# Kernel optimization log

Hardware: AMD Instinct MI355X
Metric: run time of the kernel (lower is better)

The kernel has to match this reference:

```python
import jax, jax.numpy as jnp
import numpy as np

B, T, D = 32, 512, 1024


def setup_inputs() -> dict:
    key = jax.random.key(0)
    ks = jax.random.split(key, 10)
    s = 1.0 / np.sqrt(D)
    return {
        "x": jax.random.normal(ks[0], (B, T, D), jnp.float32),
        "W1": jax.random.normal(ks[1], (D, D), jnp.float32) * s,
        "b1": jax.random.normal(ks[2], (D,), jnp.float32) * s,
        "W2": jax.random.normal(ks[3], (D, D), jnp.float32) * s,
        "b2": jax.random.normal(ks[4], (D,), jnp.float32) * s,
        "W3": jax.random.normal(ks[5], (D, D), jnp.float32) * s,
        "b3": jax.random.normal(ks[6], (D,), jnp.float32) * s,
        "W4": jax.random.normal(ks[7], (D, D), jnp.float32) * s,
        "b4": jax.random.normal(ks[8], (D,), jnp.float32) * s,
        "bias": jax.random.normal(ks[9], (1, D), jnp.float32),
    }


def _lstm(x, W1, b1, W2, b2, W3, b3, W4, b4, bias):
    # Fuse the four D->D gate projections into one [D,4D] matmul per step.
    # nn.Linear computes s @ W^T + b; weights here are stored as [out,in]=[D,D].
    Wcat = jnp.concatenate([W1.T, W2.T, W3.T, W4.T], axis=1)        # [D, 4D]
    bcat = jnp.concatenate([b1, b2, b3, b4]) + jnp.tile(bias[0], 4)  # [4D]

    def step(carry, xt):
        c, h = carry                      # cellState (hiddenUp), hidden (hiddenDown): [B,D]
        s = h + xt                        # sum_ = hiddenDown + xt
        z = s @ Wcat + bcat               # [B,4D]
        zf, zi, zg, zo = jnp.split(z, 4, axis=1)
        f = jax.nn.sigmoid(zf)            # forgetGate
        i = jax.nn.sigmoid(zi) * jnp.tanh(zg)  # inputGate
        c = c * f + i                     # cellUpdate
        h = jax.nn.sigmoid(zo) * jnp.tanh(c)   # outputGate -> hiddenDown
        return (c, h), h

    c0 = jnp.zeros((x.shape[0], x.shape[2]), x.dtype)
    h0 = jnp.zeros_like(c0)
    (cT, hT), ys = jax.lax.scan(step, (c0, h0), jnp.swapaxes(x, 0, 1))
    out = jnp.swapaxes(ys, 0, 1)          # [B,T,D]
    return out, cT[:, None, :], hT[:, None, :]


def reference(x, W1, b1, W2, b2, W3, b3, W4, b4, bias):
    return _lstm(x, W1, b1, W2, b2, W3, b3, W4, b4, bias)
```

## Files before the change

kernel.cpp:

```cpp
#include <hip/hip_runtime.h>
#include <hip/hip_bf16.h>

#define NBLK 64
#define NTHR 256

typedef __attribute__((ext_vector_type(8))) short short8;
typedef __attribute__((ext_vector_type(4))) float f32x4;

constexpr int B = 32, T = 512, D = 1024;
constexpr int JW = D / NBLK;
constexpr int KW = D / 4;
static_assert(JW * NBLK == D, "partition");


__device__ __forceinline__ unsigned short f2bf(float f) {
  unsigned u = __builtin_bit_cast(unsigned, f);
  u += 0x7FFFu + ((u >> 16) & 1u);
  return (unsigned short)(u >> 16);
}

__device__ __forceinline__ float sigm(float v) {
  return 1.0f / (1.0f + __expf(-v));
}

__device__ __forceinline__ float tanh_fast(float v) {
  v = fminf(fmaxf(v, -30.0f), 30.0f);
  float e = __expf(2.0f * v);
  return (e - 1.0f) / (e + 1.0f);
}

__device__ __forceinline__ void st_u32_llc(unsigned* p, unsigned v) {
  asm volatile("global_store_dword %0, %1, off sc0 sc1" :: "v"(p), "v"(v) : "memory");
}

struct u32x4s { unsigned x, y, z, w; };

__global__ void __launch_bounds__(NTHR, 1) lstm_persistent(
    const float* __restrict__ x,
    const float* __restrict__ W1, const float* __restrict__ b1,
    const float* __restrict__ W2, const float* __restrict__ b2,
    const float* __restrict__ W3, const float* __restrict__ b3,
    const float* __restrict__ W4, const float* __restrict__ b4,
    const float* __restrict__ bias,
    float* __restrict__ out,
    unsigned* __restrict__ flags,
    unsigned* __restrict__ sq)
{
  __shared__ float zx[2][4][B][72];

  const int blk  = blockIdx.x;
  const int tid  = threadIdx.x;
  const int wv   = tid >> 6;
  const int lane = tid & 63;
  const int j0   = blk * JW;
  const int rot  = blk & 7;

  const int m     = lane & 15;
  const int kg    = (lane >> 4) * 8;
  const int kbase = wv * KW;

  const float* Wg[4] = {W1, W2, W3, W4};
  short8 bfrag[4][8];
#pragma unroll
  for (int g = 0; g < 4; ++g) {
    const float* wrow = Wg[g] + (size_t)(j0 + m) * D + kbase;
#pragma unroll
    for (int kk = 0; kk < 8; ++kk) {
      const int kkr = (kk + rot) & 7;
      float4 fa = *(const float4*)(wrow + kkr * 32 + kg);
      float4 fb = *(const float4*)(wrow + kkr * 32 + kg + 4);
      short8 v;
      v[0] = (short)f2bf(fa.x); v[1] = (short)f2bf(fa.y);
      v[2] = (short)f2bf(fa.z); v[3] = (short)f2bf(fa.w);
      v[4] = (short)f2bf(fb.x); v[5] = (short)f2bf(fb.y);
      v[6] = (short)f2bf(fb.z); v[7] = (short)f2bf(fb.w);
      bfrag[g][kk] = v;
    }
  }

  const int gb   = tid >> 3;
  const int jp   = (tid & 7) * 2;
  const int jcol = j0 + jp;

  const float bsum0 = bias[jcol], bsum1 = bias[jcol + 1];
  const float bf0 = b1[jcol] + bsum0, bf1 = b1[jcol + 1] + bsum1;
  const float bi0 = b2[jcol] + bsum0, bi1 = b2[jcol + 1] + bsum1;
  const float bg0 = b3[jcol] + bsum0, bg1 = b3[jcol + 1] + bsum1;
  const float bo0 = b4[jcol] + bsum0, bo1 = b4[jcol + 1] + bsum1;

  const float* xrow = x + (size_t)gb * T * D + jcol;
  float* outrow     = out + (size_t)gb * T * D + jcol;
  float* cTp        = out + (size_t)B * T * D + (size_t)gb * D + jcol;
  float* hTp        = cTp + (size_t)B * D;

  {
    float2 x0 = *(const float2*)xrow;
    unsigned v = ((unsigned)f2bf(x0.x) | ((unsigned)f2bf(x0.y) << 16)) & ~1u;
    st_u32_llc(sq + blk * 256 + tid, v);
    asm volatile("s_waitcnt vmcnt(0)" ::: "memory");
    if (lane < 8) st_u32_llc(flags + lane * 256 + 4 * blk + wv, 1u);
  }

  const int aoff = ((kbase >> 4) + (kg >> 4)) * 512 + m * 16 + (kg & 8);
  const unsigned* pollp = flags + rot * 256 + 64 * wv + lane;

  float c0 = 0.0f, c1 = 0.0f;
  unsigned rA = 0, rB = 0;

  for (int t = 0; t < T; ++t) {
    const int tn = (t + 1 < T) ? (t + 1) : (T - 1);
    float2 xv;
    asm volatile("global_load_dwordx2 %0, %1, off"
                 : "=v"(xv) : "v"(xrow + (size_t)tn * D));

    {
      const unsigned tgt = (unsigned)(t + 1);
      int guard = 0;
      asm volatile("global_load_dword %0, %1, off sc0 sc1" : "=v"(rA) : "v"(pollp));
      for (;;) {
        asm volatile("global_load_dword %0, %1, off sc0 sc1" : "=v"(rB) : "v"(pollp));
        asm volatile("s_waitcnt vmcnt(1)" ::: "memory");
        __builtin_amdgcn_sched_barrier(0);
        if (__all((int)(rA >= tgt))) break;
        asm volatile("global_load_dword %0, %1, off sc0 sc1" : "=v"(rA) : "v"(pollp));
        asm volatile("s_waitcnt vmcnt(1)" ::: "memory");
        __builtin_amdgcn_sched_barrier(0);
        if (__all((int)(rB >= tgt))) break;
        if (++guard > (1 << 21)) break;
      }
    }
    __builtin_amdgcn_sched_barrier(0);

    const unsigned short* ap =
        (const unsigned short*)sq + (size_t)(t & 1) * 32768 + aoff;
    const unsigned eexp = (unsigned)(t >> 1) & 1u;
    short8 a0[8], a1[8];
    f32x4 acc[2][4];
    int atry = 0;
    bool good;
    do {
#pragma unroll
      for (int kk = 0; kk < 8; ++kk) {
        const int kkr = (kk + rot) & 7;
        asm volatile("global_load_dwordx4 %0, %1, off sc0 sc1"
                     : "=v"(a0[kk]) : "v"(ap + kkr * 1024));
        asm volatile("global_load_dwordx4 %0, %1, off sc0 sc1"
                     : "=v"(a1[kk]) : "v"(ap + kkr * 1024 + 256));
      }
#pragma unroll
      for (int mt = 0; mt < 2; ++mt)
#pragma unroll
        for (int g = 0; g < 4; ++g) acc[mt][g] = (f32x4){0.f, 0.f, 0.f, 0.f};

      unsigned orv = 0u, andv = 0xFFFFFFFFu;
#define MFMA_KK(kk, NSTR)                                                     \
      asm volatile("s_waitcnt vmcnt(" NSTR ")" ::: "memory");                 \
      __builtin_amdgcn_sched_barrier(0);                                      \
      _Pragma("unroll")                                                       \
      for (int g = 0; g < 4; ++g) {                                           \
        acc[0][g] = __builtin_amdgcn_mfma_f32_16x16x32_bf16(a0[kk], bfrag[g][kk], acc[0][g], 0, 0, 0); \
        acc[1][g] = __builtin_amdgcn_mfma_f32_16x16x32_bf16(a1[kk], bfrag[g][kk], acc[1][g], 0, 0, 0); \
      }                                                                       \
      {                                                                       \
        u32x4s q0 = __builtin_bit_cast(u32x4s, a0[kk]);                       \
        u32x4s q1 = __builtin_bit_cast(u32x4s, a1[kk]);                       \
        unsigned o_ = q0.x | q0.y | q0.z | q0.w | q1.x | q1.y | q1.z | q1.w;  \
        unsigned a_ = q0.x & q0.y & q0.z & q0.w & q1.x & q1.y & q1.z & q1.w;  \
        orv |= o_; andv &= a_;                                                \
      }
      MFMA_KK(0, "14") MFMA_KK(1, "12") MFMA_KK(2, "10") MFMA_KK(3, "8")
      MFMA_KK(4, "6")  MFMA_KK(5, "4")  MFMA_KK(6, "2")  MFMA_KK(7, "0")
#undef MFMA_KK
      const unsigned bad = eexp ? (~andv & 1u) : (orv & 1u);
      good = __all((int)(bad == 0u));
    } while (!good && ++atry < 64);

    const int pz = t & 1;
    {
      const int zr = (lane >> 4) * 4;
#pragma unroll
      for (int g = 0; g < 4; ++g)
#pragma unroll
        for (int r = 0; r < 4; ++r) {
          zx[pz][wv][zr + r][g * 16 + m]      = acc[0][g][r];
          zx[pz][wv][zr + r + 16][g * 16 + m] = acc[1][g][r];
        }
    }
    __syncthreads();

    float zf0, zf1, zi0, zi1, zg0, zg1, zo0, zo1;
    {
      float2 f_ = *(const float2*)&zx[pz][0][gb][jp];
      float2 i_ = *(const float2*)&zx[pz][0][gb][16 + jp];
      float2 g_ = *(const float2*)&zx[pz][0][gb][32 + jp];
      float2 o_ = *(const float2*)&zx[pz][0][gb][48 + jp];
      zf0 = f_.x; zf1 = f_.y; zi0 = i_.x; zi1 = i_.y;
      zg0 = g_.x; zg1 = g_.y; zo0 = o_.x; zo1 = o_.y;
#pragma unroll
      for (int w = 1; w < 4; ++w) {
        f_ = *(const float2*)&zx[pz][w][gb][jp];
        i_ = *(const float2*)&zx[pz][w][gb][16 + jp];
        g_ = *(const float2*)&zx[pz][w][gb][32 + jp];
        o_ = *(const float2*)&zx[pz][w][gb][48 + jp];
        zf0 += f_.x; zf1 += f_.y; zi0 += i_.x; zi1 += i_.y;
        zg0 += g_.x; zg1 += g_.y; zo0 += o_.x; zo1 += o_.y;
      }
    }

    float f0 = sigm(zf0 + bf0), f1 = sigm(zf1 + bf1);
    float i0 = sigm(zi0 + bi0) * tanh_fast(zg0 + bg0);
    float i1 = sigm(zi1 + bi1) * tanh_fast(zg1 + bg1);
    c0 = c0 * f0 + i0;
    c1 = c1 * f1 + i1;
    float h0 = sigm(zo0 + bo0) * tanh_fast(c0);
    float h1 = sigm(zo1 + bo1) * tanh_fast(c1);

    if (t + 1 < T) {
      const unsigned epub = (unsigned)((t + 1) >> 1) & 1u;
      unsigned v = (((unsigned)f2bf(h0 + xv.x) |
                     ((unsigned)f2bf(h1 + xv.y) << 16)) & ~1u) | epub;
      st_u32_llc(sq + (size_t)((t + 1) & 1) * 16384 + blk * 256 + tid, v);
      if (lane < 8) st_u32_llc(flags + lane * 256 + 4 * blk + wv, (unsigned)(t + 2));
      *(float2*)(outrow + (size_t)t * D) = make_float2(h0, h1);
    } else {
      *(float2*)(outrow + (size_t)t * D) = make_float2(h0, h1);
      *(float2*)cTp = make_float2(c0, c1);
      *(float2*)hTp = make_float2(h0, h1);
    }

    asm volatile("" :: "v"(rA), "v"(rB), "v"(xv));
  }
}

extern "C" void kernel_launch(void* const* d_in, const int* in_sizes, int n_in,
                              void* d_out, int out_size, void* d_ws, size_t ws_size,
                              hipStream_t stream) {
  const float* x    = (const float*)d_in[0];
  const float* W1   = (const float*)d_in[1];
  const float* b1   = (const float*)d_in[2];
  const float* W2   = (const float*)d_in[3];
  const float* b2   = (const float*)d_in[4];
  const float* W3   = (const float*)d_in[5];
  const float* b3   = (const float*)d_in[6];
  const float* W4   = (const float*)d_in[7];
  const float* b4   = (const float*)d_in[8];
  const float* bias = (const float*)d_in[9];

  unsigned* flags = (unsigned*)d_ws;
  unsigned* sq    = (unsigned*)((char*)d_ws + 8192);

  hipMemsetAsync(d_ws, 0, 8192, stream);
  hipMemsetAsync((char*)d_ws + 8192, 0xFF, 131072, stream);
  hipLaunchKernelGGL(lstm_persistent, dim3(NBLK), dim3(NTHR), 0, stream,
                     x, W1, b1, W2, b2, W3, b3, W4, b4, bias,
                     (float*)d_out, flags, sq);
}
```

Before: 1.691 ms.

## Replace flag polling with double-buffered data polling using embedded epoch bits

Removes the separate per-step flag array and its polling loop. Each block now speculatively issues two rounds of loads of the shared hidden-state buffer and checks the epoch bit embedded in every bf16 pair, retrying until one set is complete, then runs the MFMAs on that set. This removes one global round-trip (flag store and flag poll) from the serial critical path of each timestep. In exchange it roughly doubles the vector registers held for operands and adds more L2 polling traffic. An odd `zo0*0.0f` term is also added to h1, which looks like a scheduling nudge and changes nothing numerically for finite inputs.

```diff
diff --git a/kernel.cpp b/kernel.cpp
--- a/kernel.cpp
+++ b/kernel.cpp
@@ -34,6 +34,30 @@
 }
 
 struct u32x4s { unsigned x, y, z, w; };
+
+__device__ __forceinline__ int check_set(const short8* a0, const short8* a1,
+                                         unsigned eexp) {
+  unsigned r;
+  if (eexp) {
+    r = 0xFFFFFFFFu;
+#pragma unroll
+    for (int kk = 0; kk < 8; ++kk) {
+      u32x4s q0 = __builtin_bit_cast(u32x4s, a0[kk]);
+      u32x4s q1 = __builtin_bit_cast(u32x4s, a1[kk]);
+      r &= q0.x & q0.y & q0.z & q0.w & q1.x & q1.y & q1.z & q1.w;
+    }
+    return __all((int)(r & 1u));
+  } else {
+    r = 0u;
+#pragma unroll
+    for (int kk = 0; kk < 8; ++kk) {
+      u32x4s q0 = __builtin_bit_cast(u32x4s, a0[kk]);
+      u32x4s q1 = __builtin_bit_cast(u32x4s, a1[kk]);
+      r |= q0.x | q0.y | q0.z | q0.w | q1.x | q1.y | q1.z | q1.w;
+    }
+    return __all((int)((r & 1u) == 0u));
+  }
+}
 
 __global__ void __launch_bounds__(NTHR, 1) lstm_persistent(
     const float* __restrict__ x,
@@ -43,7 +67,6 @@
     const float* __restrict__ W4, const float* __restrict__ b4,
     const float* __restrict__ bias,
     float* __restrict__ out,
-    unsigned* __restrict__ flags,
     unsigned* __restrict__ sq)
 {
   __shared__ float zx[2][4][B][72];
@@ -97,15 +120,35 @@
     float2 x0 = *(const float2*)xrow;
     unsigned v = ((unsigned)f2bf(x0.x) | ((unsigned)f2bf(x0.y) << 16)) & ~1u;
     st_u32_llc(sq + blk * 256 + tid, v);
-    asm volatile("s_waitcnt vmcnt(0)" ::: "memory");
-    if (lane < 8) st_u32_llc(flags + lane * 256 + 4 * blk + wv, 1u);
   }
 
   const int aoff = ((kbase >> 4) + (kg >> 4)) * 512 + m * 16 + (kg & 8);
-  const unsigned* pollp = flags + rot * 256 + 64 * wv + lane;
 
   float c0 = 0.0f, c1 = 0.0f;
-  unsigned rA = 0, rB = 0;
+  short8 a0A[8], a1A[8], a0B[8], a1B[8];
+
+#define ISSUE_SET(A0, A1)                                                     \
+  do {                                                                        \
+    _Pragma("unroll")                                                         \
+    for (int kk = 0; kk < 8; ++kk) {                                          \
+      const int kkr = (kk + rot) & 7;                                         \
+      asm volatile("global_load_dwordx4 %0, %1, off sc0 sc1"                  \
+                   : "=v"((A0)[kk]) : "v"(ap + kkr * 1024));                  \
+      asm volatile("global_load_dwordx4 %0, %1, off sc0 sc1"                  \
+                   : "=v"((A1)[kk]) : "v"(ap + kkr * 1024 + 256));            \
+    }                                                                         \
+  } while (0)
+
+#define MFMA_ALL(A0, A1)                                                      \
+  do {                                                                        \
+    _Pragma("unroll")                                                         \
+    for (int kk = 0; kk < 8; ++kk)                                            \
+      _Pragma("unroll")                                                       \
+      for (int g = 0; g < 4; ++g) {                                           \
+        acc[0][g] = __builtin_amdgcn_mfma_f32_16x16x32_bf16((A0)[kk], bfrag[g][kk], acc[0][g], 0, 0, 0); \
+        acc[1][g] = __builtin_amdgcn_mfma_f32_16x16x32_bf16((A1)[kk], bfrag[g][kk], acc[1][g], 0, 0, 0); \
+      }                                                                       \
+  } while (0)
 
   for (int t = 0; t < T; ++t) {
     const int tn = (t + 1 < T) ? (t + 1) : (T - 1);
@@ -113,67 +156,33 @@
     asm volatile("global_load_dwordx2 %0, %1, off"
                  : "=v"(xv) : "v"(xrow + (size_t)tn * D));
 
-    {
-      const unsigned tgt = (unsigned)(t + 1);
-      int guard = 0;
-      asm volatile("global_load_dword %0, %1, off sc0 sc1" : "=v"(rA) : "v"(pollp));
-      for (;;) {
-        asm volatile("global_load_dword %0, %1, off sc0 sc1" : "=v"(rB) : "v"(pollp));
-        asm volatile("s_waitcnt vmcnt(1)" ::: "memory");
-        __builtin_amdgcn_sched_barrier(0);
-        if (__all((int)(rA >= tgt))) break;
-        asm volatile("global_load_dword %0, %1, off sc0 sc1" : "=v"(rA) : "v"(pollp));
-        asm volatile("s_waitcnt vmcnt(1)" ::: "memory");
-        __builtin_amdgcn_sched_barrier(0);
-        if (__all((int)(rB >= tgt))) break;
-        if (++guard > (1 << 21)) break;
-      }
-    }
-    __builtin_amdgcn_sched_barrier(0);
-
     const unsigned short* ap =
         (const unsigned short*)sq + (size_t)(t & 1) * 32768 + aoff;
     const unsigned eexp = (unsigned)(t >> 1) & 1u;
-    short8 a0[8], a1[8];
+
+    ISSUE_SET(a0A, a1A);
+    ISSUE_SET(a0B, a1B);
+    int sel = 0, guard = 0;
+    for (;;) {
+      asm volatile("s_waitcnt vmcnt(16)" ::: "memory");
+      __builtin_amdgcn_sched_barrier(0);
+      if (check_set(a0A, a1A, eexp)) { sel = 0; break; }
+      ISSUE_SET(a0A, a1A);
+      asm volatile("s_waitcnt vmcnt(16)" ::: "memory");
+      __builtin_amdgcn_sched_barrier(0);
+      if (check_set(a0B, a1B, eexp)) { sel = 1; break; }
+      ISSUE_SET(a0B, a1B);
+      if (++guard > (1 << 18)) { sel = 0; break; }
+    }
+    __builtin_amdgcn_sched_barrier(0);
+
     f32x4 acc[2][4];
-    int atry = 0;
-    bool good;
-    do {
-#pragma unroll
-      for (int kk = 0; kk < 8; ++kk) {
-        const int kkr = (kk + rot) & 7;
-        asm volatile("global_load_dwordx4 %0, %1, off sc0 sc1"
-                     : "=v"(a0[kk]) : "v"(ap + kkr * 1024));
-        asm volatile("global_load_dwordx4 %0, %1, off sc0 sc1"
-                     : "=v"(a1[kk]) : "v"(ap + kkr * 1024 + 256));
-      }
-#pragma unroll
-      for (int mt = 0; mt < 2; ++mt)
-#pragma unroll
-        for (int g = 0; g < 4; ++g) acc[mt][g] = (f32x4){0.f, 0.f, 0.f, 0.f};
-
-      unsigned orv = 0u, andv = 0xFFFFFFFFu;
-#define MFMA_KK(kk, NSTR)                                                     \
-      asm volatile("s_waitcnt vmcnt(" NSTR ")" ::: "memory");                 \
-      __builtin_amdgcn_sched_barrier(0);                                      \
-      _Pragma("unroll")                                                       \
-      for (int g = 0; g < 4; ++g) {                                           \
-        acc[0][g] = __builtin_amdgcn_mfma_f32_16x16x32_bf16(a0[kk], bfrag[g][kk], acc[0][g], 0, 0, 0); \
-        acc[1][g] = __builtin_amdgcn_mfma_f32_16x16x32_bf16(a1[kk], bfrag[g][kk], acc[1][g], 0, 0, 0); \
-      }                                                                       \
-      {                                                                       \
-        u32x4s q0 = __builtin_bit_cast(u32x4s, a0[kk]);                       \
-        u32x4s q1 = __builtin_bit_cast(u32x4s, a1[kk]);                       \
-        unsigned o_ = q0.x | q0.y | q0.z | q0.w | q1.x | q1.y | q1.z | q1.w;  \
-        unsigned a_ = q0.x & q0.y & q0.z & q0.w & q1.x & q1.y & q1.z & q1.w;  \
-        orv |= o_; andv &= a_;                                                \
-      }
-      MFMA_KK(0, "14") MFMA_KK(1, "12") MFMA_KK(2, "10") MFMA_KK(3, "8")
-      MFMA_KK(4, "6")  MFMA_KK(5, "4")  MFMA_KK(6, "2")  MFMA_KK(7, "0")
-#undef MFMA_KK
-      const unsigned bad = eexp ? (~andv & 1u) : (orv & 1u);
-      good = __all((int)(bad == 0u));
-    } while (!good && ++atry < 64);
+#pragma unroll
+    for (int mt = 0; mt < 2; ++mt)
+#pragma unroll
+      for (int g = 0; g < 4; ++g) acc[mt][g] = (f32x4){0.f, 0.f, 0.f, 0.f};
+    if (sel == 0) MFMA_ALL(a0A, a1A);
+    else          MFMA_ALL(a0B, a1B);
 
     const int pz = t & 1;
     {
@@ -213,14 +222,13 @@
     c0 = c0 * f0 + i0;
     c1 = c1 * f1 + i1;
     float h0 = sigm(zo0 + bo0) * tanh_fast(c0);
-    float h1 = sigm(zo1 + bo1) * tanh_fast(c1);
+    float h1 = sigm(zo0 * 0.0f + zo1 + bo1) * tanh_fast(c1);
 
     if (t + 1 < T) {
       const unsigned epub = (unsigned)((t + 1) >> 1) & 1u;
       unsigned v = (((unsigned)f2bf(h0 + xv.x) |
                      ((unsigned)f2bf(h1 + xv.y) << 16)) & ~1u) | epub;
       st_u32_llc(sq + (size_t)((t + 1) & 1) * 16384 + blk * 256 + tid, v);
-      if (lane < 8) st_u32_llc(flags + lane * 256 + 4 * blk + wv, (unsigned)(t + 2));
       *(float2*)(outrow + (size_t)t * D) = make_float2(h0, h1);
     } else {
       *(float2*)(outrow + (size_t)t * D) = make_float2(h0, h1);
@@ -228,8 +236,13 @@
       *(float2*)hTp = make_float2(h0, h1);
     }
 
-    asm volatile("" :: "v"(rA), "v"(rB), "v"(xv));
-  }
+#pragma unroll
+    for (int kk = 0; kk < 8; ++kk)
+      asm volatile("" :: "v"(a0A[kk]), "v"(a1A[kk]), "v"(a0B[kk]), "v"(a1B[kk]));
+    asm volatile("" :: "v"(xv));
+  }
+#undef ISSUE_SET
+#undef MFMA_ALL
 }
 
 extern "C" void kernel_launch(void* const* d_in, const int* in_sizes, int n_in,
@@ -246,12 +259,10 @@
   const float* b4   = (const float*)d_in[8];
   const float* bias = (const float*)d_in[9];
 
-  unsigned* flags = (unsigned*)d_ws;
-  unsigned* sq    = (unsigned*)((char*)d_ws + 8192);
-
-  hipMemsetAsync(d_ws, 0, 8192, stream);
-  hipMemsetAsync((char*)d_ws + 8192, 0xFF, 131072, stream);
+  unsigned* sq = (unsigned*)d_ws;
+
+  hipMemsetAsync(d_ws, 0xFF, 131072, stream);
   hipLaunchKernelGGL(lstm_persistent, dim3(NBLK), dim3(NTHR), 0, stream,
                      x, W1, b1, W2, b2, W3, b3, W4, b4, bias,
-                     (float*)d_out, flags, sq);
-}
+                     (float*)d_out, sq);
+}
```

Result: faster. 1.602 ms (-5.3%).
